# Kernel optimization log

Hardware: AMD Instinct MI355X
Metric: run time of the kernel (lower is better)

## Reference

```python
import jax, jax.numpy as jnp
import numpy as np

D = 1024
H = 16
HD = D // H
EPS = 1e-5


def layer_norm(x, g, b):
    mu = jnp.mean(x, axis=-1, keepdims=True)
    var = jnp.mean((x - mu) ** 2, axis=-1, keepdims=True)
    return (x - mu) * jax.lax.rsqrt(var + EPS) * g + b


def setup_inputs() -> dict:
    key = jax.random.key(0)
    ks = jax.random.split(key, 10)
    s = lambda fan_in: 1.0 / np.sqrt(fan_in)
    inp = {
        "x": jax.random.normal(ks[0], (2, 2048, D), dtype=jnp.float32),
        "w_qkv": jax.random.uniform(ks[1], (D, 3 * D), minval=-s(D), maxval=s(D)),
        "b_qkv": jnp.zeros((3 * D,), jnp.float32),
        "w_fc": jax.random.uniform(ks[2], (D, D), minval=-s(D), maxval=s(D)),
        "b_fc": jnp.zeros((D,), jnp.float32),
        "ln1_g": jnp.ones((D,), jnp.float32),
        "ln1_b": jnp.zeros((D,), jnp.float32),
        "ln2_g": jnp.ones((D,), jnp.float32),
        "ln2_b": jnp.zeros((D,), jnp.float32),
        "w1": jax.random.uniform(ks[3], (D, 4 * D), minval=-s(D), maxval=s(D)),
        "b1": jnp.zeros((4 * D,), jnp.float32),
        "w2": jax.random.uniform(ks[4], (4 * D, D), minval=-s(4 * D), maxval=s(4 * D)),
        "b2": jnp.zeros((D,), jnp.float32),
    }
    return inp


def reference(x, w_qkv, b_qkv, w_fc, b_fc, ln1_g, ln1_b, ln2_g, ln2_b, w1, b1, w2, b2):
    B, T, C = x.shape
    # --- attention sublayer (pre-norm) ---
    h = layer_norm(x, ln1_g, ln1_b)
    qkv = (h @ w_qkv + b_qkv).reshape(B, T, 3, H, HD)
    q, k, v = qkv[:, :, 0], qkv[:, :, 1], qkv[:, :, 2]  # [B,T,H,HD]
    scores = jnp.einsum("bqhd,bkhd->bhqk", q, k) / np.sqrt(HD).astype(np.float32)
    causal = jnp.tril(jnp.ones((T, T), dtype=bool))
    scores = jnp.where(causal, scores, -jnp.inf)
    weights = jax.nn.softmax(scores, axis=-1)
    out = jnp.einsum("bhqk,bkhd->bqhd", weights, v).reshape(B, T, C)
    x = x + out @ w_fc + b_fc
    # --- MLP sublayer (pre-norm) ---
    h = layer_norm(x, ln2_g, ln2_b)
    h = jax.nn.gelu(h @ w1 + b1, approximate=False) @ w2 + b2
    return x + h
```

## Files before the change

kernel.cpp:

```cpp
#include <hip/hip_runtime.h>
#include <hip/hip_bf16.h>
#include <cstdint>
#include <cstddef>

#define SEQ 2048
#define DM  1024

typedef __attribute__((ext_vector_type(8))) __bf16 bf16x8;
typedef __attribute__((ext_vector_type(4))) float  f32x4;
using bf16 = __hip_bfloat16;

__device__ __forceinline__ void gload_lds16(const bf16* g, bf16* l) {
  __builtin_amdgcn_global_load_lds((const __attribute__((address_space(1))) void*)g,
                                   (__attribute__((address_space(3))) void*)l,
                                   16, 0, 0);
}

__global__ void transpose_to_bf16(const float* __restrict__ in, bf16* __restrict__ out,
                                  int K, int N) {
  __shared__ float tile[32][33];
  const int k0 = blockIdx.y * 32, n0 = blockIdx.x * 32;
  const int tx = threadIdx.x, ty = threadIdx.y;
#pragma unroll
  for (int i = ty; i < 32; i += 8)
    tile[i][tx] = in[(size_t)(k0 + i) * N + n0 + tx];
  __syncthreads();
#pragma unroll
  for (int i = ty; i < 32; i += 8)
    out[(size_t)(n0 + i) * K + k0 + tx] = __float2bfloat16(tile[tx][i]);
}

__global__ void ln_to_bf16(const float* __restrict__ x, const float* __restrict__ g,
                           const float* __restrict__ bt, bf16* __restrict__ out) {
  const int row = blockIdx.x;
  const float4 v = ((const float4*)(x + (size_t)row * DM))[threadIdx.x];
  float s  = v.x + v.y + v.z + v.w;
  float s2 = v.x * v.x + v.y * v.y + v.z * v.z + v.w * v.w;
#pragma unroll
  for (int o = 32; o > 0; o >>= 1) { s += __shfl_down(s, o); s2 += __shfl_down(s2, o); }
  __shared__ float red[8];
  const int wave = threadIdx.x >> 6, lane = threadIdx.x & 63;
  if (lane == 0) { red[wave] = s; red[4 + wave] = s2; }
  __syncthreads();
  s  = red[0] + red[1] + red[2] + red[3];
  s2 = red[4] + red[5] + red[6] + red[7];
  const float mu  = s * (1.f / DM);
  const float var = s2 * (1.f / DM) - mu * mu;
  const float r   = rsqrtf(var + 1e-5f);
  const float4 gv = ((const float4*)g)[threadIdx.x];
  const float4 bv = ((const float4*)bt)[threadIdx.x];
  bf16* o = out + (size_t)row * DM + threadIdx.x * 4;
  o[0] = __float2bfloat16((v.x - mu) * r * gv.x + bv.x);
  o[1] = __float2bfloat16((v.y - mu) * r * gv.y + bv.y);
  o[2] = __float2bfloat16((v.z - mu) * r * gv.z + bv.z);
  o[3] = __float2bfloat16((v.w - mu) * r * gv.w + bv.w);
}

enum { EP_BF16 = 0, EP_GELU = 1, EP_RESID = 2 };

template <int MODE, int TN>
__global__ void gemm_bt(const bf16* __restrict__ A, const bf16* __restrict__ Bt,
                        const float* __restrict__ bias, const float* __restrict__ resid,
                        float* __restrict__ Cf, bf16* __restrict__ Cb,
                        int M, int N, int K) {
  constexpr int ABUF = 128 * 32;
  constexpr int BBUF = TN * 32;
  constexpr int NI = TN / 32;
  __shared__ __attribute__((aligned(16))) bf16 As[2 * ABUF];
  __shared__ __attribute__((aligned(16))) bf16 Bs[2 * BBUF];
  const int tid  = threadIdx.x;
  const int wave = tid >> 6, lane = tid & 63;
  const int l16 = lane & 15, lq = lane >> 4;
  const int m0 = blockIdx.x * 128, n0 = blockIdx.y * TN;
  const int wr = (wave >> 1) * 64, wc = (wave & 1) * (TN / 2);

  f32x4 acc[4][NI];
#pragma unroll
  for (int i = 0; i < 4; i++)
#pragma unroll
    for (int j = 0; j < NI; j++) acc[i][j] = 0;

  const int srow = tid >> 2;
  const int scol = (tid & 3) * 8;
  const bf16* ga = A  + (size_t)(m0 + srow) * K + scol;
  const bf16* gb = Bt + (size_t)(n0 + srow) * K + scol;

  {
    bf16* la = As + wave * 512;
    bf16* lb = Bs + wave * 512;
    gload_lds16(ga, la);
    gload_lds16(ga + (size_t)64 * K, la + 2048);
    gload_lds16(gb, lb);
    if (TN == 128) gload_lds16(gb + (size_t)64 * K, lb + 2048);
  }

  const int NKT = K >> 5;
  for (int it = 0; it < NKT; ++it) {
    __syncthreads();
    const int cur = it & 1, nxt = cur ^ 1;
    if (it + 1 < NKT) {
      const int kt = (it + 1) << 5;
      bf16* la = As + nxt * ABUF + wave * 512;
      bf16* lb = Bs + nxt * BBUF + wave * 512;
      gload_lds16(ga + kt, la);
      gload_lds16(ga + (size_t)64 * K + kt, la + 2048);
      gload_lds16(gb + kt, lb);
      if (TN == 128) gload_lds16(gb + (size_t)64 * K + kt, lb + 2048);
    }
    bf16x8 af[4], bfr[NI];
#pragma unroll
    for (int mi = 0; mi < 4; mi++)
      af[mi] = *(const bf16x8*)(As + cur * ABUF + (wr + mi * 16 + l16) * 32 + lq * 8);
#pragma unroll
    for (int ni = 0; ni < NI; ni++)
      bfr[ni] = *(const bf16x8*)(Bs + cur * BBUF + (wc + ni * 16 + l16) * 32 + lq * 8);
#pragma unroll
    for (int mi = 0; mi < 4; mi++)
#pragma unroll
      for (int ni = 0; ni < NI; ni++)
        acc[mi][ni] = __builtin_amdgcn_mfma_f32_16x16x32_bf16(af[mi], bfr[ni], acc[mi][ni], 0, 0, 0);
  }

#pragma unroll
  for (int ni = 0; ni < NI; ni++) {
    const int col = n0 + wc + ni * 16 + l16;
    const float bb = bias[col];
#pragma unroll
    for (int mi = 0; mi < 4; mi++) {
#pragma unroll
      for (int r = 0; r < 4; r++) {
        const int row = m0 + wr + mi * 16 + lq * 4 + r;
        const size_t idx = (size_t)row * N + col;
        float v = acc[mi][ni][r] + bb;
        if (MODE == EP_BF16) {
          Cb[idx] = __float2bfloat16(v);
        } else if (MODE == EP_GELU) {
          v = 0.5f * v * (1.0f + erff(v * 0.70710678118654752f));
          Cb[idx] = __float2bfloat16(v);
        } else {
          Cf[idx] = resid[idx] + v;
        }
      }
    }
  }
}

#define SCALE_LOG2 0.18033688011112042f

__global__ void flash_attn(const bf16* __restrict__ qkv, bf16* __restrict__ out) {
  const int id = blockIdx.x;
  const int a  = id & 7;
  const int h  = (id >> 3) & 15;
  const int b  = (id >> 7) & 1;
  const int m  = (id >> 8) & 3;
  const int qb = a ^ (((m & 1) * 15) | ((m & 2) << 3));

  const int tid = threadIdx.x;
  const int w = tid >> 6, lane = tid & 63;
  const int l16 = lane & 15, lq = lane >> 4;

  const size_t base = (size_t)b * SEQ * 3072;
  const bf16* Qg = qkv + base + (size_t)h * 64;
  const bf16* Kg = qkv + base + 1024 + (size_t)h * 64;
  const ushort* Vg = (const ushort*)(qkv + base + 2048 + (size_t)h * 64);

  __shared__ __attribute__((aligned(16))) bf16 Qs[64][72];
  __shared__ __attribute__((aligned(16))) bf16 Ks[64][72];
  __shared__ __attribute__((aligned(16))) bf16 VTs[64 * 64];
  __shared__ __attribute__((aligned(16))) bf16 Ps[4][16][72];

  const int q0 = qb * 64;
  const int nkb = qb + 1;

  const int krow = tid >> 2, kcol = (tid & 3) * 16;
  const int vd = tid & 63, vc = tid >> 6;
  const int vsw0 = ((vc ^ (vd & 7)) * 8);
  const int vsw1 = (((vc + 4) ^ (vd & 7)) * 8);

  {
    const int r = tid >> 2, c = (tid & 3) * 16;
    const bf16* src = Qg + (size_t)(q0 + r) * 3072 + c;
    *(uint4*)(&Qs[r][c])     = *(const uint4*)(src);
    *(uint4*)(&Qs[r][c + 8]) = *(const uint4*)(src + 8);

    const bf16* ks = Kg + (size_t)krow * 3072 + kcol;
    const uint4 k0 = *(const uint4*)(ks);
    const uint4 k1 = *(const uint4*)(ks + 8);
    ushort va[8], vb[8];
#pragma unroll
    for (int j = 0; j < 8; j++) va[j] = Vg[(size_t)(vc * 8 + j) * 3072 + vd];
#pragma unroll
    for (int j = 0; j < 8; j++) vb[j] = Vg[(size_t)((vc + 4) * 8 + j) * 3072 + vd];
    *(uint4*)(&Ks[krow][kcol])     = k0;
    *(uint4*)(&Ks[krow][kcol + 8]) = k1;
    uint4 wa, wb;
    wa.x = (uint)va[0] | ((uint)va[1] << 16); wa.y = (uint)va[2] | ((uint)va[3] << 16);
    wa.z = (uint)va[4] | ((uint)va[5] << 16); wa.w = (uint)va[6] | ((uint)va[7] << 16);
    wb.x = (uint)vb[0] | ((uint)vb[1] << 16); wb.y = (uint)vb[2] | ((uint)vb[3] << 16);
    wb.z = (uint)vb[4] | ((uint)vb[5] << 16); wb.w = (uint)vb[6] | ((uint)vb[7] << 16);
    *(uint4*)(&VTs[vd * 64 + vsw0]) = wa;
    *(uint4*)(&VTs[vd * 64 + vsw1]) = wb;
  }
  __syncthreads();

  const bf16x8 qf0 = *(const bf16x8*)(&Qs[w * 16 + l16][lq * 8]);
  const bf16x8 qf1 = *(const bf16x8*)(&Qs[w * 16 + l16][32 + lq * 8]);

  f32x4 oacc[4];
#pragma unroll
  for (int i = 0; i < 4; i++) oacc[i] = 0;
  float lsum[4] = {0.f, 0.f, 0.f, 0.f};

  uint4 kr0, kr1;
  ushort va[8], vb[8];
  const int sw0 = (lq ^ (l16 & 7)) * 8;
  const int sw1 = ((4 + lq) ^ (l16 & 7)) * 8;

  for (int kb = 0; kb < nkb; ++kb) {
    const bool more = (kb + 1 < nkb);

    if (more) {
      const size_t koff = (size_t)((kb + 1) * 64);
      const bf16* ks = Kg + (koff + krow) * 3072 + kcol;
      kr0 = *(const uint4*)(ks);
      kr1 = *(const uint4*)(ks + 8);
#pragma unroll
      for (int j = 0; j < 8; j++) va[j] = Vg[(koff + vc * 8 + j) * 3072 + vd];
#pragma unroll
      for (int j = 0; j < 8; j++) vb[j] = Vg[(koff + (vc + 4) * 8 + j) * 3072 + vd];
    }

    f32x4 sacc[4];
#pragma unroll
    for (int nt = 0; nt < 4; nt++) sacc[nt] = 0;
#pragma unroll
    for (int nt = 0; nt < 4; nt++) {
      const bf16x8 kf0 = *(const bf16x8*)(&Ks[nt * 16 + l16][lq * 8]);
      const bf16x8 kf1 = *(const bf16x8*)(&Ks[nt * 16 + l16][32 + lq * 8]);
      sacc[nt] = __builtin_amdgcn_mfma_f32_16x16x32_bf16(qf0, kf0, sacc[nt], 0, 0, 0);
      sacc[nt] = __builtin_amdgcn_mfma_f32_16x16x32_bf16(qf1, kf1, sacc[nt], 0, 0, 0);
    }

    const bool diag = (kb == qb);
#pragma unroll
    for (int r = 0; r < 4; r++) {
      float e[4];
#pragma unroll
      for (int nt = 0; nt < 4; nt++) {
        float sv = sacc[nt][r] * SCALE_LOG2;
        sv = fminf(sv, 88.f);
        if (diag && (nt * 16 + l16 > w * 16 + lq * 4 + r)) sv = -1e30f;
        e[nt] = exp2f(sv);
        Ps[w][lq * 4 + r][nt * 16 + l16] = __float2bfloat16(e[nt]);
      }
      lsum[r] += (e[0] + e[1]) + (e[2] + e[3]);
    }

    const bf16x8 pf0 = *(const bf16x8*)(&Ps[w][l16][lq * 8]);
    const bf16x8 pf1 = *(const bf16x8*)(&Ps[w][l16][32 + lq * 8]);
#pragma unroll
    for (int dt = 0; dt < 4; dt++) {
      const int d = dt * 16 + l16;
      const bf16x8 vf0 = *(const bf16x8*)(&VTs[d * 64 + sw0]);
      const bf16x8 vf1 = *(const bf16x8*)(&VTs[d * 64 + sw1]);
      oacc[dt] = __builtin_amdgcn_mfma_f32_16x16x32_bf16(pf0, vf0, oacc[dt], 0, 0, 0);
      oacc[dt] = __builtin_amdgcn_mfma_f32_16x16x32_bf16(pf1, vf1, oacc[dt], 0, 0, 0);
    }

    if (more) {
      __syncthreads();
      *(uint4*)(&Ks[krow][kcol])     = kr0;
      *(uint4*)(&Ks[krow][kcol + 8]) = kr1;
      uint4 wa, wb;
      wa.x = (uint)va[0] | ((uint)va[1] << 16); wa.y = (uint)va[2] | ((uint)va[3] << 16);
      wa.z = (uint)va[4] | ((uint)va[5] << 16); wa.w = (uint)va[6] | ((uint)va[7] << 16);
      wb.x = (uint)vb[0] | ((uint)vb[1] << 16); wb.y = (uint)vb[2] | ((uint)vb[3] << 16);
      wb.z = (uint)vb[4] | ((uint)vb[5] << 16); wb.w = (uint)vb[6] | ((uint)vb[7] << 16);
      *(uint4*)(&VTs[vd * 64 + vsw0]) = wa;
      *(uint4*)(&VTs[vd * 64 + vsw1]) = wb;
      __syncthreads();
    }
  }

#pragma unroll
  for (int r = 0; r < 4; r++) {
    float l = lsum[r];
    l += __shfl_xor(l, 1);
    l += __shfl_xor(l, 2);
    l += __shfl_xor(l, 4);
    l += __shfl_xor(l, 8);
    lsum[r] = 1.f / l;
  }
#pragma unroll
  for (int dt = 0; dt < 4; dt++)
#pragma unroll
    for (int r = 0; r < 4; r++) {
      const int qrow = q0 + w * 16 + lq * 4 + r;
      const float v = oacc[dt][r] * lsum[r];
      out[(size_t)(b * SEQ + qrow) * DM + h * 64 + dt * 16 + l16] = __float2bfloat16(v);
    }
}

extern "C" void kernel_launch(void* const* d_in, const int* in_sizes, int n_in,
                              void* d_out, int out_size, void* d_ws, size_t ws_size,
                              hipStream_t stream) {
  const float* x     = (const float*)d_in[0];
  const float* w_qkv = (const float*)d_in[1];
  const float* b_qkv = (const float*)d_in[2];
  const float* w_fc  = (const float*)d_in[3];
  const float* b_fc  = (const float*)d_in[4];
  const float* ln1_g = (const float*)d_in[5];
  const float* ln1_b = (const float*)d_in[6];
  const float* ln2_g = (const float*)d_in[7];
  const float* ln2_b = (const float*)d_in[8];
  const float* w1    = (const float*)d_in[9];
  const float* b1    = (const float*)d_in[10];
  const float* w2    = (const float*)d_in[11];
  const float* b2    = (const float*)d_in[12];
  float* out = (float*)d_out;

  char* ws    = (char*)d_ws;
  float* x2   = (float*)(ws);
  bf16* big   = (bf16*)(ws + (size_t)(16 << 20));
  bf16* small = (bf16*)(ws + (size_t)(48 << 20));
  bf16* wT    = (bf16*)(ws + (size_t)(56 << 20));

  const dim3 tb(32, 8);

  ln_to_bf16<<<dim3(4096), dim3(256), 0, stream>>>(x, ln1_g, ln1_b, small);
  transpose_to_bf16<<<dim3(96, 32), tb, 0, stream>>>(w_qkv, wT, 1024, 3072);
  gemm_bt<EP_BF16, 128><<<dim3(32, 24), dim3(256), 0, stream>>>(
      small, wT, b_qkv, nullptr, nullptr, big, 4096, 3072, 1024);
  flash_attn<<<dim3(1024), dim3(256), 0, stream>>>(big, small);
  transpose_to_bf16<<<dim3(32, 32), tb, 0, stream>>>(w_fc, wT, 1024, 1024);
  gemm_bt<EP_RESID, 64><<<dim3(32, 16), dim3(256), 0, stream>>>(
      small, wT, b_fc, x, x2, nullptr, 4096, 1024, 1024);
  ln_to_bf16<<<dim3(4096), dim3(256), 0, stream>>>(x2, ln2_g, ln2_b, small);
  transpose_to_bf16<<<dim3(128, 32), tb, 0, stream>>>(w1, wT, 1024, 4096);
  gemm_bt<EP_GELU, 128><<<dim3(32, 32), dim3(256), 0, stream>>>(
      small, wT, b1, nullptr, nullptr, big, 4096, 4096, 1024);
  transpose_to_bf16<<<dim3(32, 128), tb, 0, stream>>>(w2, wT, 4096, 1024);
  gemm_bt<EP_RESID, 64><<<dim3(32, 16), dim3(256), 0, stream>>>(
      big, wT, b2, x2, out, nullptr, 4096, 1024, 4096);
}
```

Before: 383.6 us.

## Write V transposed from QKV GEMM and stream K/V into LDS asynchronously

The QKV GEMM epilogue now writes the V section transposed (head-dim major, sequence contiguous) into a workspace buffer. This lets flash attention load K and V tiles with direct global-to-LDS 16-byte loads into double-buffered, XOR-swizzled shared memory, replacing the strided per-element V gathers and register staging. Q fragments are read straight from global memory, P uses a swizzled layout, and the diagonal block has its own masked path. In exchange the GEMM does narrower strided stores for V, and the V buffer reuses the x2 workspace region before x2 is written.

```diff
diff --git a/kernel.cpp b/kernel.cpp
--- a/kernel.cpp
+++ b/kernel.cpp
@@ -56,12 +56,12 @@
   o[3] = __float2bfloat16((v.w - mu) * r * gv.w + bv.w);
 }
 
-enum { EP_BF16 = 0, EP_GELU = 1, EP_RESID = 2 };
+enum { EP_BF16 = 0, EP_GELU = 1, EP_RESID = 2, EP_QKV = 3 };
 
 template <int MODE, int TN>
 __global__ void gemm_bt(const bf16* __restrict__ A, const bf16* __restrict__ Bt,
                         const float* __restrict__ bias, const float* __restrict__ resid,
-                        float* __restrict__ Cf, bf16* __restrict__ Cb,
+                        float* __restrict__ Cf, bf16* __restrict__ Cb, bf16* __restrict__ vt,
                         int M, int N, int K) {
   constexpr int ABUF = 128 * 32;
   constexpr int BBUF = TN * 32;
@@ -127,18 +127,33 @@
     const float bb = bias[col];
 #pragma unroll
     for (int mi = 0; mi < 4; mi++) {
-#pragma unroll
-      for (int r = 0; r < 4; r++) {
-        const int row = m0 + wr + mi * 16 + lq * 4 + r;
-        const size_t idx = (size_t)row * N + col;
-        float v = acc[mi][ni][r] + bb;
-        if (MODE == EP_BF16) {
-          Cb[idx] = __float2bfloat16(v);
-        } else if (MODE == EP_GELU) {
-          v = 0.5f * v * (1.0f + erff(v * 0.70710678118654752f));
-          Cb[idx] = __float2bfloat16(v);
+      if constexpr (MODE == EP_QKV) {
+        const int row0 = m0 + wr + mi * 16 + lq * 4;
+        if (col >= 2048) {
+          __attribute__((aligned(8))) bf16 pk[4];
+#pragma unroll
+          for (int r = 0; r < 4; r++) pk[r] = __float2bfloat16(acc[mi][ni][r] + bb);
+          *(uint2*)(vt + (size_t)((row0 >> 11) * 1024 + (col - 2048)) * SEQ + (row0 & 2047)) =
+              *(const uint2*)pk;
         } else {
-          Cf[idx] = resid[idx] + v;
+#pragma unroll
+          for (int r = 0; r < 4; r++)
+            Cb[(size_t)(row0 + r) * N + col] = __float2bfloat16(acc[mi][ni][r] + bb);
+        }
+      } else {
+#pragma unroll
+        for (int r = 0; r < 4; r++) {
+          const int row = m0 + wr + mi * 16 + lq * 4 + r;
+          const size_t idx = (size_t)row * N + col;
+          float v = acc[mi][ni][r] + bb;
+          if (MODE == EP_BF16) {
+            Cb[idx] = __float2bfloat16(v);
+          } else if (MODE == EP_GELU) {
+            v = 0.5f * v * (1.0f + erff(v * 0.70710678118654752f));
+            Cb[idx] = __float2bfloat16(v);
+          } else {
+            Cf[idx] = resid[idx] + v;
+          }
         }
       }
     }
@@ -147,7 +162,9 @@
 
 #define SCALE_LOG2 0.18033688011112042f
 
-__global__ void flash_attn(const bf16* __restrict__ qkv, bf16* __restrict__ out) {
+__global__ __launch_bounds__(256, 4)
+void flash_attn(const bf16* __restrict__ qkv, const bf16* __restrict__ VTg,
+                bf16* __restrict__ out) {
   const int id = blockIdx.x;
   const int a  = id & 7;
   const int h  = (id >> 3) & 15;
@@ -162,72 +179,53 @@
   const size_t base = (size_t)b * SEQ * 3072;
   const bf16* Qg = qkv + base + (size_t)h * 64;
   const bf16* Kg = qkv + base + 1024 + (size_t)h * 64;
-  const ushort* Vg = (const ushort*)(qkv + base + 2048 + (size_t)h * 64);
-
-  __shared__ __attribute__((aligned(16))) bf16 Qs[64][72];
-  __shared__ __attribute__((aligned(16))) bf16 Ks[64][72];
-  __shared__ __attribute__((aligned(16))) bf16 VTs[64 * 64];
-  __shared__ __attribute__((aligned(16))) bf16 Ps[4][16][72];
+  const bf16* Vt = VTg + (size_t)(b * 1024 + h * 64) * SEQ;
+
+  __shared__ __attribute__((aligned(16))) bf16 Ks[2 * 4096];
+  __shared__ __attribute__((aligned(16))) bf16 VTs[2 * 4096];
+  __shared__ __attribute__((aligned(16))) bf16 Ps[4 * 1024];
 
   const int q0 = qb * 64;
   const int nkb = qb + 1;
 
-  const int krow = tid >> 2, kcol = (tid & 3) * 16;
-  const int vd = tid & 63, vc = tid >> 6;
-  const int vsw0 = ((vc ^ (vd & 7)) * 8);
-  const int vsw1 = (((vc + 4) ^ (vd & 7)) * 8);
-
-  {
-    const int r = tid >> 2, c = (tid & 3) * 16;
-    const bf16* src = Qg + (size_t)(q0 + r) * 3072 + c;
-    *(uint4*)(&Qs[r][c])     = *(const uint4*)(src);
-    *(uint4*)(&Qs[r][c + 8]) = *(const uint4*)(src + 8);
-
-    const bf16* ks = Kg + (size_t)krow * 3072 + kcol;
-    const uint4 k0 = *(const uint4*)(ks);
-    const uint4 k1 = *(const uint4*)(ks + 8);
-    ushort va[8], vb[8];
-#pragma unroll
-    for (int j = 0; j < 8; j++) va[j] = Vg[(size_t)(vc * 8 + j) * 3072 + vd];
-#pragma unroll
-    for (int j = 0; j < 8; j++) vb[j] = Vg[(size_t)((vc + 4) * 8 + j) * 3072 + vd];
-    *(uint4*)(&Ks[krow][kcol])     = k0;
-    *(uint4*)(&Ks[krow][kcol + 8]) = k1;
-    uint4 wa, wb;
-    wa.x = (uint)va[0] | ((uint)va[1] << 16); wa.y = (uint)va[2] | ((uint)va[3] << 16);
-    wa.z = (uint)va[4] | ((uint)va[5] << 16); wa.w = (uint)va[6] | ((uint)va[7] << 16);
-    wb.x = (uint)vb[0] | ((uint)vb[1] << 16); wb.y = (uint)vb[2] | ((uint)vb[3] << 16);
-    wb.z = (uint)vb[4] | ((uint)vb[5] << 16); wb.w = (uint)vb[6] | ((uint)vb[7] << 16);
-    *(uint4*)(&VTs[vd * 64 + vsw0]) = wa;
-    *(uint4*)(&VTs[vd * 64 + vsw1]) = wb;
-  }
-  __syncthreads();
-
-  const bf16x8 qf0 = *(const bf16x8*)(&Qs[w * 16 + l16][lq * 8]);
-  const bf16x8 qf1 = *(const bf16x8*)(&Qs[w * 16 + l16][32 + lq * 8]);
+  const int srow = tid >> 3;
+  const int scb  = (tid & 7) ^ (srow & 7);
+  const bf16* gK0 = Kg + (size_t)srow * 3072 + scb * 8;
+  const bf16* gK1 = Kg + (size_t)(srow + 32) * 3072 + scb * 8;
+  const bf16* gV0 = Vt + (size_t)srow * SEQ + scb * 8;
+  const bf16* gV1 = Vt + (size_t)(srow + 32) * SEQ + scb * 8;
+  const int ldst0 = w * 512;
+  const int ldst1 = 2048 + w * 512;
+
+  gload_lds16(gK0, Ks + ldst0);
+  gload_lds16(gK1, Ks + ldst1);
+  gload_lds16(gV0, VTs + ldst0);
+  gload_lds16(gV1, VTs + ldst1);
+
+  const bf16* qrow = Qg + (size_t)(q0 + w * 16 + l16) * 3072 + lq * 8;
+  const bf16x8 qf0 = *(const bf16x8*)(qrow);
+  const bf16x8 qf1 = *(const bf16x8*)(qrow + 32);
+
+  const int koffA = l16 * 64 + ((lq ^ (l16 & 7)) << 3);
+  const int koffB = l16 * 64 + (((4 + lq) ^ (l16 & 7)) << 3);
+  const int l16h = l16 >> 3;
+  const int pco  = w * 1024 + (l16 & 7);
 
   f32x4 oacc[4];
 #pragma unroll
   for (int i = 0; i < 4; i++) oacc[i] = 0;
   float lsum[4] = {0.f, 0.f, 0.f, 0.f};
 
-  uint4 kr0, kr1;
-  ushort va[8], vb[8];
-  const int sw0 = (lq ^ (l16 & 7)) * 8;
-  const int sw1 = ((4 + lq) ^ (l16 & 7)) * 8;
-
   for (int kb = 0; kb < nkb; ++kb) {
-    const bool more = (kb + 1 < nkb);
-
-    if (more) {
-      const size_t koff = (size_t)((kb + 1) * 64);
-      const bf16* ks = Kg + (koff + krow) * 3072 + kcol;
-      kr0 = *(const uint4*)(ks);
-      kr1 = *(const uint4*)(ks + 8);
-#pragma unroll
-      for (int j = 0; j < 8; j++) va[j] = Vg[(koff + vc * 8 + j) * 3072 + vd];
-#pragma unroll
-      for (int j = 0; j < 8; j++) vb[j] = Vg[(koff + (vc + 4) * 8 + j) * 3072 + vd];
+    __syncthreads();
+    const int cur = (kb & 1) * 4096;
+    if (kb + 1 < nkb) {
+      const int nxt = ((kb + 1) & 1) * 4096;
+      const size_t ko = (size_t)(kb + 1) * 64;
+      gload_lds16(gK0 + ko * 3072, Ks + nxt + ldst0);
+      gload_lds16(gK1 + ko * 3072, Ks + nxt + ldst1);
+      gload_lds16(gV0 + ko, VTs + nxt + ldst0);
+      gload_lds16(gV1 + ko, VTs + nxt + ldst1);
     }
 
     f32x4 sacc[4];
@@ -235,50 +233,52 @@
     for (int nt = 0; nt < 4; nt++) sacc[nt] = 0;
 #pragma unroll
     for (int nt = 0; nt < 4; nt++) {
-      const bf16x8 kf0 = *(const bf16x8*)(&Ks[nt * 16 + l16][lq * 8]);
-      const bf16x8 kf1 = *(const bf16x8*)(&Ks[nt * 16 + l16][32 + lq * 8]);
+      const bf16x8 kf0 = *(const bf16x8*)(Ks + cur + nt * 1024 + koffA);
+      const bf16x8 kf1 = *(const bf16x8*)(Ks + cur + nt * 1024 + koffB);
       sacc[nt] = __builtin_amdgcn_mfma_f32_16x16x32_bf16(qf0, kf0, sacc[nt], 0, 0, 0);
       sacc[nt] = __builtin_amdgcn_mfma_f32_16x16x32_bf16(qf1, kf1, sacc[nt], 0, 0, 0);
     }
 
-    const bool diag = (kb == qb);
-#pragma unroll
-    for (int r = 0; r < 4; r++) {
-      float e[4];
-#pragma unroll
-      for (int nt = 0; nt < 4; nt++) {
-        float sv = sacc[nt][r] * SCALE_LOG2;
-        sv = fminf(sv, 88.f);
-        if (diag && (nt * 16 + l16 > w * 16 + lq * 4 + r)) sv = -1e30f;
-        e[nt] = exp2f(sv);
-        Ps[w][lq * 4 + r][nt * 16 + l16] = __float2bfloat16(e[nt]);
+    if (kb == qb) {
+#pragma unroll
+      for (int r = 0; r < 4; r++) {
+        const int rowp = lq * 4 + r;
+        const int qloc = w * 16 + rowp;
+        float e[4];
+#pragma unroll
+        for (int nt = 0; nt < 4; nt++) {
+          float sv = sacc[nt][r] * SCALE_LOG2;
+          sv = fminf(sv, 88.f);
+          if (nt * 16 + l16 > qloc) sv = -1e30f;
+          e[nt] = exp2f(sv);
+          Ps[pco + rowp * 64 + ((((nt * 2 + l16h)) ^ (rowp & 7)) << 3)] = __float2bfloat16(e[nt]);
+        }
+        lsum[r] += (e[0] + e[1]) + (e[2] + e[3]);
       }
-      lsum[r] += (e[0] + e[1]) + (e[2] + e[3]);
-    }
-
-    const bf16x8 pf0 = *(const bf16x8*)(&Ps[w][l16][lq * 8]);
-    const bf16x8 pf1 = *(const bf16x8*)(&Ps[w][l16][32 + lq * 8]);
+    } else {
+#pragma unroll
+      for (int r = 0; r < 4; r++) {
+        const int rowp = lq * 4 + r;
+        float e[4];
+#pragma unroll
+        for (int nt = 0; nt < 4; nt++) {
+          float sv = sacc[nt][r] * SCALE_LOG2;
+          sv = fminf(sv, 88.f);
+          e[nt] = exp2f(sv);
+          Ps[pco + rowp * 64 + ((((nt * 2 + l16h)) ^ (rowp & 7)) << 3)] = __float2bfloat16(e[nt]);
+        }
+        lsum[r] += (e[0] + e[1]) + (e[2] + e[3]);
+      }
+    }
+
+    const bf16x8 pf0 = *(const bf16x8*)(Ps + w * 1024 + koffA);
+    const bf16x8 pf1 = *(const bf16x8*)(Ps + w * 1024 + koffB);
 #pragma unroll
     for (int dt = 0; dt < 4; dt++) {
-      const int d = dt * 16 + l16;
-      const bf16x8 vf0 = *(const bf16x8*)(&VTs[d * 64 + sw0]);
-      const bf16x8 vf1 = *(const bf16x8*)(&VTs[d * 64 + sw1]);
+      const bf16x8 vf0 = *(const bf16x8*)(VTs + cur + dt * 1024 + koffA);
+      const bf16x8 vf1 = *(const bf16x8*)(VTs + cur + dt * 1024 + koffB);
       oacc[dt] = __builtin_amdgcn_mfma_f32_16x16x32_bf16(pf0, vf0, oacc[dt], 0, 0, 0);
       oacc[dt] = __builtin_amdgcn_mfma_f32_16x16x32_bf16(pf1, vf1, oacc[dt], 0, 0, 0);
-    }
-
-    if (more) {
-      __syncthreads();
-      *(uint4*)(&Ks[krow][kcol])     = kr0;
-      *(uint4*)(&Ks[krow][kcol + 8]) = kr1;
-      uint4 wa, wb;
-      wa.x = (uint)va[0] | ((uint)va[1] << 16); wa.y = (uint)va[2] | ((uint)va[3] << 16);
-      wa.z = (uint)va[4] | ((uint)va[5] << 16); wa.w = (uint)va[6] | ((uint)va[7] << 16);
-      wb.x = (uint)vb[0] | ((uint)vb[1] << 16); wb.y = (uint)vb[2] | ((uint)vb[3] << 16);
-      wb.z = (uint)vb[4] | ((uint)vb[5] << 16); wb.w = (uint)vb[6] | ((uint)vb[7] << 16);
-      *(uint4*)(&VTs[vd * 64 + vsw0]) = wa;
-      *(uint4*)(&VTs[vd * 64 + vsw1]) = wb;
-      __syncthreads();
     }
   }
 
@@ -295,9 +295,9 @@
   for (int dt = 0; dt < 4; dt++)
 #pragma unroll
     for (int r = 0; r < 4; r++) {
-      const int qrow = q0 + w * 16 + lq * 4 + r;
+      const int qrow_ = q0 + w * 16 + lq * 4 + r;
       const float v = oacc[dt][r] * lsum[r];
-      out[(size_t)(b * SEQ + qrow) * DM + h * 64 + dt * 16 + l16] = __float2bfloat16(v);
+      out[(size_t)(b * SEQ + qrow_) * DM + h * 64 + dt * 16 + l16] = __float2bfloat16(v);
     }
 }
 
@@ -321,6 +321,7 @@
 
   char* ws    = (char*)d_ws;
   float* x2   = (float*)(ws);
+  bf16* VTg   = (bf16*)(ws);
   bf16* big   = (bf16*)(ws + (size_t)(16 << 20));
   bf16* small = (bf16*)(ws + (size_t)(48 << 20));
   bf16* wT    = (bf16*)(ws + (size_t)(56 << 20));
@@ -329,17 +330,17 @@
 
   ln_to_bf16<<<dim3(4096), dim3(256), 0, stream>>>(x, ln1_g, ln1_b, small);
   transpose_to_bf16<<<dim3(96, 32), tb, 0, stream>>>(w_qkv, wT, 1024, 3072);
-  gemm_bt<EP_BF16, 128><<<dim3(32, 24), dim3(256), 0, stream>>>(
-      small, wT, b_qkv, nullptr, nullptr, big, 4096, 3072, 1024);
-  flash_attn<<<dim3(1024), dim3(256), 0, stream>>>(big, small);
+  gemm_bt<EP_QKV, 128><<<dim3(32, 24), dim3(256), 0, stream>>>(
+      small, wT, b_qkv, nullptr, nullptr, big, VTg, 4096, 3072, 1024);
+  flash_attn<<<dim3(1024), dim3(256), 0, stream>>>(big, VTg, small);
   transpose_to_bf16<<<dim3(32, 32), tb, 0, stream>>>(w_fc, wT, 1024, 1024);
   gemm_bt<EP_RESID, 64><<<dim3(32, 16), dim3(256), 0, stream>>>(
-      small, wT, b_fc, x, x2, nullptr, 4096, 1024, 1024);
+      small, wT, b_fc, x, x2, nullptr, nullptr, 4096, 1024, 1024);
   ln_to_bf16<<<dim3(4096), dim3(256), 0, stream>>>(x2, ln2_g, ln2_b, small);
   transpose_to_bf16<<<dim3(128, 32), tb, 0, stream>>>(w1, wT, 1024, 4096);
   gemm_bt<EP_GELU, 128><<<dim3(32, 32), dim3(256), 0, stream>>>(
-      small, wT, b1, nullptr, nullptr, big, 4096, 4096, 1024);
+      small, wT, b1, nullptr, nullptr, big, nullptr, 4096, 4096, 1024);
   transpose_to_bf16<<<dim3(32, 128), tb, 0, stream>>>(w2, wT, 4096, 1024);
   gemm_bt<EP_RESID, 64><<<dim3(32, 16), dim3(256), 0, stream>>>(
-      big, wT, b2, x2, out, nullptr, 4096, 1024, 4096);
-}
+      big, wT, b2, x2, out, nullptr, nullptr, 4096, 1024, 4096);
+}
```

Measured after the change: 371.2 us. 3.2% less time.
